# Optimization experiments

Hardware: AMD Instinct MI355X
Metric: run time of the kernel (lower is better)

## Reference

```python
import jax, jax.numpy as jnp
import numpy as np

B, T, N, U = 16, 512, 2048, 64  # batch_size, dim1, dim2 (=nodes), units


def setup_inputs() -> dict:
    key = jax.random.key(0)
    k1, k2, k3, k4 = jax.random.split(key, 4)
    x = jax.random.normal(k1, (B, T, N), dtype=jnp.float32)
    Adj = jax.random.uniform(k2, (N, N), dtype=jnp.float32)
    W = jax.random.normal(k3, (U, N), dtype=jnp.float32) * 0.05  # 'uniform' init stand-in
    b = jax.random.normal(k4, (U,), dtype=jnp.float32) * 0.05
    return {"x": x, "Adj": Adj, "W": W, "b": b}


def reference(x, Adj, W, b):
    # Original loop: out_i[b,t,j] = sum_k x[b,t,k] * Adj[j,k] * W[i,k] + b[i],
    # then mean over i. By linearity this equals a single matmul with the
    # unit-averaged weight vector and the averaged bias.
    w_bar = jnp.mean(W, axis=0)              # [N]
    w_eff = Adj * w_bar                       # [N(j), N(k)] : Adj[j,k] * w_bar[k]
    out = jnp.einsum('btk,jk->btj', x, w_eff) + jnp.mean(b)
    return out  # [B, T, N]
```

## Files before the change

kernel.cpp:

```cpp
#include <hip/hip_runtime.h>

#define N_DIM 2048
#define U_DIM 64
#define M_DIM 8192
#define K_DIM 2048

typedef __bf16 bf16x8 __attribute__((ext_vector_type(8)));
typedef float  floatx4 __attribute__((ext_vector_type(4)));
typedef unsigned short ushort8 __attribute__((ext_vector_type(8)));

#define AS1 __attribute__((address_space(1)))
#define AS3 __attribute__((address_space(3)))

__device__ __forceinline__ unsigned short f_to_bf16_rne(float f) {
    unsigned int x;
    __builtin_memcpy(&x, &f, 4);
    x += 0x7fffu + ((x >> 16) & 1u);
    return (unsigned short)(x >> 16);
}

__global__ __launch_bounds__(256) void prep_kernel(
    const float* __restrict__ W, const float* __restrict__ b,
    float* __restrict__ wbar, float* __restrict__ bmean) {
    int k = blockIdx.x * 256 + threadIdx.x;
    float s = 0.f;
#pragma unroll
    for (int i = 0; i < U_DIM; ++i) s += W[i * N_DIM + k];
    wbar[k] = s * (1.f / U_DIM);

    if (blockIdx.x == 0 && threadIdx.x < 64) {
        float v = b[threadIdx.x];
#pragma unroll
        for (int off = 32; off > 0; off >>= 1) v += __shfl_down(v, off);
        if (threadIdx.x == 0) bmean[0] = v * (1.f / U_DIM);
    }
}

__global__ __launch_bounds__(256) void weff_convx_kernel(
    const float* __restrict__ Adj, const float* __restrict__ wbar,
    unsigned short* __restrict__ weff,
    const float* __restrict__ x, unsigned short* __restrict__ xbf) {
    if (blockIdx.x < 2048) {
        long long idx = ((long long)blockIdx.x * 256 + threadIdx.x) * 8;
        int k = (int)(idx & (N_DIM - 1));
        floatx4 a0 = *(const floatx4*)(Adj + idx);
        floatx4 a1 = *(const floatx4*)(Adj + idx + 4);
        floatx4 w0 = *(const floatx4*)(wbar + k);
        floatx4 w1 = *(const floatx4*)(wbar + k + 4);
        ushort8 ov;
#pragma unroll
        for (int j = 0; j < 4; ++j) {
            ov[j]     = f_to_bf16_rne(a0[j] * w0[j]);
            ov[j + 4] = f_to_bf16_rne(a1[j] * w1[j]);
        }
        *(ushort8*)(weff + idx) = ov;
    } else {
        long long idx = ((long long)(blockIdx.x - 2048) * 256 + threadIdx.x) * 8;
        floatx4 a0 = *(const floatx4*)(x + idx);
        floatx4 a1 = *(const floatx4*)(x + idx + 4);
        ushort8 ov;
#pragma unroll
        for (int j = 0; j < 4; ++j) {
            ov[j]     = f_to_bf16_rne(a0[j]);
            ov[j + 4] = f_to_bf16_rne(a1[j]);
        }
        *(ushort8*)(xbf + idx) = ov;
    }
}

__global__ __launch_bounds__(256) void convx_kernel(
    const float* __restrict__ x, unsigned short* __restrict__ xbf) {
    long long idx = ((long long)blockIdx.x * 256 + threadIdx.x) * 8;
    floatx4 a0 = *(const floatx4*)(x + idx);
    floatx4 a1 = *(const floatx4*)(x + idx + 4);
    ushort8 ov;
#pragma unroll
    for (int j = 0; j < 4; ++j) {
        ov[j]     = f_to_bf16_rne(a0[j]);
        ov[j + 4] = f_to_bf16_rne(a1[j]);
    }
    *(ushort8*)(xbf + idx) = ov;
}

#define BM 128
#define BN 128
#define BK 64

__global__ __launch_bounds__(256) void gemm_bt_kernel(
    const unsigned short* __restrict__ A,
    const unsigned short* __restrict__ Bt,
    const float* __restrict__ bmeanp,
    float* __restrict__ C,
    int mtiles) {
    __shared__ __align__(16) unsigned short sA[BM * BK];
    __shared__ __align__(16) unsigned short sB[BN * BK];

    const int id    = blockIdx.x;
    const int xcd   = id & 7;
    const int local = id >> 3;
    const int nt    = xcd * 2 + (local & 1);
    const int mt    = local >> 1;
    const int tile_m = mt * BM;
    const int tile_n = nt * BN;

    const int tid  = threadIdx.x;
    const int w    = tid >> 6;
    const int lane = tid & 63;

    const float bmean = bmeanp[0];

    const int srow_in = lane >> 3;
    const int skc     = (lane & 7) ^ srow_in;
    const int scol    = skc * 8;
    const unsigned short* gA[4];
    const unsigned short* gB[4];
    unsigned short* lA[4];
    unsigned short* lB[4];
#pragma unroll
    for (int i = 0; i < 4; ++i) {
        int c = w * 4 + i;
        gA[i] = A  + (size_t)(tile_m + c * 8 + srow_in) * K_DIM + scol;
        gB[i] = Bt + (size_t)(tile_n + c * 8 + srow_in) * K_DIM + scol;
        lA[i] = &sA[c * 8 * BK];
        lB[i] = &sB[c * 8 * BK];
    }

    const int wrow = (w >> 1) * 64;
    const int wcol = (w & 1) * 64;
    const int fr = lane & 15;
    const int fq = lane >> 4;
    int aoff[4][2], boff[4][2];
#pragma unroll
    for (int i = 0; i < 4; ++i)
#pragma unroll
        for (int s = 0; s < 2; ++s) {
            int kc = s * 4 + fq;
            int slot = kc ^ (fr & 7);
            aoff[i][s] = (wrow + i * 16 + fr) * BK + slot * 8;
            boff[i][s] = (wcol + i * 16 + fr) * BK + slot * 8;
        }

    floatx4 acc[4][4];
#pragma unroll
    for (int mi = 0; mi < 4; ++mi)
#pragma unroll
        for (int ni = 0; ni < 4; ++ni) acc[mi][ni] = (floatx4){0.f, 0.f, 0.f, 0.f};

    for (int k0 = 0; k0 < K_DIM; k0 += BK) {
        __syncthreads();
#pragma unroll
        for (int i = 0; i < 4; ++i) {
            __builtin_amdgcn_global_load_lds((const AS1 void*)(gA[i] + k0),
                                             (AS3 void*)lA[i], 16, 0, 0);
            __builtin_amdgcn_global_load_lds((const AS1 void*)(gB[i] + k0),
                                             (AS3 void*)lB[i], 16, 0, 0);
        }
        __syncthreads();

#pragma unroll
        for (int s = 0; s < 2; ++s) {
            bf16x8 af[4], bf[4];
#pragma unroll
            for (int i = 0; i < 4; ++i) {
                af[i] = *(const bf16x8*)&sA[aoff[i][s]];
                bf[i] = *(const bf16x8*)&sB[boff[i][s]];
            }
#pragma unroll
            for (int mi = 0; mi < 4; ++mi)
#pragma unroll
                for (int ni = 0; ni < 4; ++ni)
                    acc[mi][ni] = __builtin_amdgcn_mfma_f32_16x16x32_bf16(
                        af[mi], bf[ni], acc[mi][ni], 0, 0, 0);
        }
    }

    const int crow = tile_m + wrow + fq * 4;
    const int ccol = tile_n + wcol + fr;
#pragma unroll
    for (int mi = 0; mi < 4; ++mi)
#pragma unroll
        for (int ni = 0; ni < 4; ++ni)
#pragma unroll
            for (int r = 0; r < 4; ++r) {
                int gm = crow + mi * 16 + r;
                int gn = ccol + ni * 16;
                C[(size_t)gm * N_DIM + gn] = acc[mi][ni][r] + bmean;
            }
    (void)mtiles;
}

extern "C" void kernel_launch(void* const* d_in, const int* in_sizes, int n_in,
                              void* d_out, int out_size, void* d_ws, size_t ws_size,
                              hipStream_t stream) {
    (void)in_sizes; (void)n_in; (void)out_size;
    const float* x   = (const float*)d_in[0];
    const float* Adj = (const float*)d_in[1];
    const float* W   = (const float*)d_in[2];
    const float* b   = (const float*)d_in[3];
    float* out = (float*)d_out;

    char* ws = (char*)d_ws;
    float* wbar  = (float*)ws;
    float* bmean = (float*)(ws + 8192);
    unsigned short* weff = (unsigned short*)(ws + 16384);
    const size_t weff_bytes = (size_t)N_DIM * N_DIM * 2;
    const size_t xbf_off = 16384 + weff_bytes;
    unsigned short* xbf = (unsigned short*)(ws + xbf_off);

    size_t avail = (ws_size > xbf_off) ? (ws_size - xbf_off) : 0;
    long long max_rows = (long long)(avail / ((size_t)K_DIM * 2)) / BM * BM;
    if (max_rows < BM) max_rows = BM;
    if (max_rows > M_DIM) max_rows = M_DIM;

    prep_kernel<<<N_DIM / 256, 256, 0, stream>>>(W, b, wbar, bmean);

    if (max_rows == M_DIM) {
        weff_convx_kernel<<<2048 + M_DIM, 256, 0, stream>>>(Adj, wbar, weff, x, xbf);
        gemm_bt_kernel<<<(N_DIM / BN) * (M_DIM / BM), 256, 0, stream>>>(
            xbf, weff, bmean, out, M_DIM / BM);
    } else {
        weff_convx_kernel<<<2048, 256, 0, stream>>>(Adj, wbar, weff, x, xbf);
        for (long long m0 = 0; m0 < M_DIM; m0 += max_rows) {
            long long rows = (M_DIM - m0 < max_rows) ? (M_DIM - m0) : max_rows;
            convx_kernel<<<(int)rows, 256, 0, stream>>>(x + m0 * K_DIM, xbf);
            gemm_bt_kernel<<<(N_DIM / BN) * (int)(rows / BM), 256, 0, stream>>>(
                xbf, weff, bmean, out + m0 * (size_t)N_DIM, (int)(rows / BM));
        }
    }
}
```

Measured before the change: 226.4 us.

## Load A fragments directly from global into registers with software prefetch

The A operand is no longer staged through LDS. Each wave reads its MFMA A fragments straight from global memory into registers, and the next K-step's fragments are prefetched while the current step's MFMAs run. Only B still goes through LDS. This halves LDS traffic and the LDS footprint, but each A row is now fetched by two waves (the two column-waves) instead of once per block, and the loads are less coalesced and raise register pressure.

```diff
diff --git a/kernel.cpp b/kernel.cpp
--- a/kernel.cpp
+++ b/kernel.cpp
@@ -92,7 +92,6 @@
     const float* __restrict__ bmeanp,
     float* __restrict__ C,
     int mtiles) {
-    __shared__ __align__(16) unsigned short sA[BM * BK];
     __shared__ __align__(16) unsigned short sB[BN * BK];
 
     const int id    = blockIdx.x;
@@ -112,16 +111,12 @@
     const int srow_in = lane >> 3;
     const int skc     = (lane & 7) ^ srow_in;
     const int scol    = skc * 8;
-    const unsigned short* gA[4];
     const unsigned short* gB[4];
-    unsigned short* lA[4];
     unsigned short* lB[4];
 #pragma unroll
     for (int i = 0; i < 4; ++i) {
         int c = w * 4 + i;
-        gA[i] = A  + (size_t)(tile_m + c * 8 + srow_in) * K_DIM + scol;
         gB[i] = Bt + (size_t)(tile_n + c * 8 + srow_in) * K_DIM + scol;
-        lA[i] = &sA[c * 8 * BK];
         lB[i] = &sB[c * 8 * BK];
     }
 
@@ -129,50 +124,70 @@
     const int wcol = (w & 1) * 64;
     const int fr = lane & 15;
     const int fq = lane >> 4;
-    int aoff[4][2], boff[4][2];
+
+    int boff[4][2];
 #pragma unroll
     for (int i = 0; i < 4; ++i)
 #pragma unroll
         for (int s = 0; s < 2; ++s) {
             int kc = s * 4 + fq;
             int slot = kc ^ (fr & 7);
-            aoff[i][s] = (wrow + i * 16 + fr) * BK + slot * 8;
             boff[i][s] = (wcol + i * 16 + fr) * BK + slot * 8;
         }
 
+    const unsigned short* pA[4];
+#pragma unroll
+    for (int mi = 0; mi < 4; ++mi)
+        pA[mi] = A + (size_t)(tile_m + wrow + mi * 16 + fr) * K_DIM + fq * 8;
+
     floatx4 acc[4][4];
 #pragma unroll
     for (int mi = 0; mi < 4; ++mi)
 #pragma unroll
         for (int ni = 0; ni < 4; ++ni) acc[mi][ni] = (floatx4){0.f, 0.f, 0.f, 0.f};
 
-    for (int k0 = 0; k0 < K_DIM; k0 += BK) {
-        __syncthreads();
-#pragma unroll
-        for (int i = 0; i < 4; ++i) {
-            __builtin_amdgcn_global_load_lds((const AS1 void*)(gA[i] + k0),
-                                             (AS3 void*)lA[i], 16, 0, 0);
-            __builtin_amdgcn_global_load_lds((const AS1 void*)(gB[i] + k0),
-                                             (AS3 void*)lB[i], 16, 0, 0);
-        }
-        __syncthreads();
-
-#pragma unroll
-        for (int s = 0; s < 2; ++s) {
-            bf16x8 af[4], bf[4];
-#pragma unroll
-            for (int i = 0; i < 4; ++i) {
-                af[i] = *(const bf16x8*)&sA[aoff[i][s]];
-                bf[i] = *(const bf16x8*)&sB[boff[i][s]];
-            }
-#pragma unroll
-            for (int mi = 0; mi < 4; ++mi)
-#pragma unroll
-                for (int ni = 0; ni < 4; ++ni)
-                    acc[mi][ni] = __builtin_amdgcn_mfma_f32_16x16x32_bf16(
-                        af[mi], bf[ni], acc[mi][ni], 0, 0, 0);
-        }
-    }
+    bf16x8 arA[4][2], arB[4][2];
+#pragma unroll
+    for (int mi = 0; mi < 4; ++mi) {
+        arA[mi][0] = *(const bf16x8*)(pA[mi]);
+        arA[mi][1] = *(const bf16x8*)(pA[mi] + 32);
+    }
+
+#define GEMM_STEP(K0, CUR, NXT, KPF, DO_PF)                                   \
+    {                                                                         \
+        __syncthreads();                                                      \
+        _Pragma("unroll")                                                     \
+        for (int i = 0; i < 4; ++i)                                           \
+            __builtin_amdgcn_global_load_lds((const AS1 void*)(gB[i] + (K0)), \
+                                             (AS3 void*)lB[i], 16, 0, 0);     \
+        __syncthreads();                                                      \
+        if (DO_PF) {                                                          \
+            _Pragma("unroll")                                                 \
+            for (int mi = 0; mi < 4; ++mi) {                                  \
+                NXT[mi][0] = *(const bf16x8*)(pA[mi] + (KPF));                \
+                NXT[mi][1] = *(const bf16x8*)(pA[mi] + (KPF) + 32);           \
+            }                                                                 \
+        }                                                                     \
+        _Pragma("unroll")                                                     \
+        for (int s = 0; s < 2; ++s) {                                         \
+            bf16x8 bfr[4];                                                    \
+            _Pragma("unroll")                                                 \
+            for (int i = 0; i < 4; ++i)                                       \
+                bfr[i] = *(const bf16x8*)&sB[boff[i][s]];                     \
+            _Pragma("unroll")                                                 \
+            for (int mi = 0; mi < 4; ++mi)                                    \
+                _Pragma("unroll")                                             \
+                for (int ni = 0; ni < 4; ++ni)                                \
+                    acc[mi][ni] = __builtin_amdgcn_mfma_f32_16x16x32_bf16(    \
+                        CUR[mi][s], bfr[ni], acc[mi][ni], 0, 0, 0);           \
+        }                                                                     \
+    }
+
+    for (int k0 = 0; k0 < K_DIM; k0 += 2 * BK) {
+        GEMM_STEP(k0, arA, arB, k0 + BK, 1);
+        GEMM_STEP(k0 + BK, arB, arA, k0 + 2 * BK, (k0 + 2 * BK < K_DIM));
+    }
+#undef GEMM_STEP
 
     const int crow = tile_m + wrow + fq * 4;
     const int ccol = tile_n + wcol + fr;
```

Result: slower. 299.5 us (+32.3%).
